# Performance work log

Measured on AMD Instinct MI355X. Metric: run time of the kernel, lower is better.

Reference implementation:

```python
import jax, jax.numpy as jnp
import numpy as np

P, H, T, B = 16, 24, 168, 4096


def _lstm(x, W_ih, W_hh, b_ih, b_hh):
    # x: [B, T, F]; PyTorch gate order i, f, g, o; returns all hidden states [B, T, H]
    Bsz = x.shape[0]
    Hd = W_hh.shape[1]
    # batch the input GEMM over all timesteps
    xg = jnp.einsum('btf,gf->btg', x, W_ih) + b_ih + b_hh  # [B, T, 4H]

    def step(carry, xt):
        h, c = carry
        g = xt + h @ W_hh.T  # [B, 4H]
        i, f, gg, o = jnp.split(g, 4, axis=-1)
        c = jax.nn.sigmoid(f) * c + jax.nn.sigmoid(i) * jnp.tanh(gg)
        h = jax.nn.sigmoid(o) * jnp.tanh(c)
        return (h, c), h

    h0 = jnp.zeros((Bsz, Hd), x.dtype)
    _, hs = jax.lax.scan(step, (h0, h0), jnp.swapaxes(xg, 0, 1))
    return jnp.swapaxes(hs, 0, 1)  # [B, T, H]


def setup_inputs() -> dict:
    key = jax.random.key(0)
    ks = jax.random.split(key, 14)
    s1 = 1.0 / np.sqrt(H)
    u = lambda k, shape: jax.random.uniform(k, shape, jnp.float32, -s1, s1)
    return {
        'x': jax.random.normal(ks[0], (B, T, P), jnp.float32),
        'W_ih1': u(ks[1], (4 * H, P)), 'W_hh1': u(ks[2], (4 * H, H)),
        'b_ih1': u(ks[3], (4 * H,)), 'b_hh1': u(ks[4], (4 * H,)),
        'W_ih2': u(ks[5], (4 * H, H)), 'W_hh2': u(ks[6], (4 * H, H)),
        'b_ih2': u(ks[7], (4 * H,)), 'b_hh2': u(ks[8], (4 * H,)),
        'W1': u(ks[9], (16, H)), 'b1': u(ks[10], (16,)),
        'W2': u(ks[11], (H, 16)), 'b2': u(ks[12], (H,)),
    }


def reference(x, W_ih1, W_hh1, b_ih1, b_hh1, W_ih2, W_hh2, b_ih2, b_hh2, W1, b1, W2, b2):
    h = jnp.tanh(_lstm(x, W_ih1, W_hh1, b_ih1, b_hh1))       # [B, T, H]
    h = jnp.tanh(_lstm(h, W_ih2, W_hh2, b_ih2, b_hh2))       # [B, T, H]
    h = h[:, -1, :]                                           # [B, H]
    h = jax.nn.relu(h @ W1.T + b1)                            # [B, 16]; dropout = identity (eval mode)
    out = h @ W2.T + b2                                       # [B, 24]
    return out.reshape(out.shape[0], -1, 1)                   # [B, 24, 1]
```

## Files before the change

### kernel.cpp

```cpp
#include <hip/hip_runtime.h>

constexpr int T = 168;
constexpr int P = 16;
constexpr int H = 24;

typedef float v2f __attribute__((ext_vector_type(2)));

__device__ __forceinline__ v2f mk2(float a, float b) { v2f r; r[0] = a; r[1] = b; return r; }
__device__ __forceinline__ v2f bc2(float a)          { v2f r; r[0] = a; r[1] = a; return r; }
__device__ __forceinline__ v2f pkfma(v2f a, v2f b, v2f c) {
    return __builtin_elementwise_fma(a, b, c);
}

__device__ __forceinline__ float rcp_f(float x) { return __builtin_amdgcn_rcpf(x); }
__device__ __forceinline__ float sigm_f(float x) { return rcp_f(1.f + __expf(-x)); }
__device__ __forceinline__ float tanh_fast(float x) {
    return fmaf(2.f, rcp_f(1.f + __expf(-2.f * x)), -1.f);
}

#define KEEP2(v) asm volatile("" : "+v"(v))
#define LDS_SYNC() asm volatile("s_waitcnt lgkmcnt(0)" ::: "memory")

__global__ __attribute__((amdgpu_flat_work_group_size(64, 64),
                          amdgpu_waves_per_eu(2, 2)))
void lstm2_pk(const float* __restrict__ x,
              const float* __restrict__ Wih1, const float* __restrict__ Whh1,
              const float* __restrict__ bih1, const float* __restrict__ bhh1,
              const float* __restrict__ Wih2, const float* __restrict__ Whh2,
              const float* __restrict__ bih2, const float* __restrict__ bhh2,
              const float* __restrict__ W1, const float* __restrict__ b1,
              const float* __restrict__ W2, const float* __restrict__ b2,
              float* __restrict__ out)
{
    const int lane = threadIdx.x;
    const int s    = (lane < 48) ? lane : 47;
    const int u    = s % H;
    const int half = s / H;
    const int q0   = half * H + u;
    const int q1   = (2 + half) * H + u;
    const int rowA = blockIdx.x * 2;
    const int rowB = rowA + 1;

    v2f wx[P];
    v2f wh[H];
    v2f vx[H];
    v2f vh[H];
    #pragma unroll
    for (int k = 0; k < P; ++k) wx[k] = mk2(Wih1[q0 * P + k], Wih1[q1 * P + k]);
    #pragma unroll
    for (int k = 0; k < H; ++k) wh[k] = mk2(Whh1[q0 * H + k], Whh1[q1 * H + k]);
    #pragma unroll
    for (int k = 0; k < H; ++k) vx[k] = mk2(Wih2[q0 * H + k], Wih2[q1 * H + k]);
    #pragma unroll
    for (int k = 0; k < H; ++k) vh[k] = mk2(Whh2[q0 * H + k], Whh2[q1 * H + k]);
    v2f bias1 = mk2(bih1[q0] + bhh1[q0], bih1[q1] + bhh1[q1]);
    v2f bias2 = mk2(bih2[q0] + bhh2[q0], bih2[q1] + bhh2[q1]);

    #pragma unroll
    for (int k = 0; k < P; ++k) KEEP2(wx[k]);
    #pragma unroll
    for (int k = 0; k < H; ++k) { KEEP2(wh[k]); KEEP2(vx[k]); KEEP2(vh[k]); }
    KEEP2(bias1); KEEP2(bias2);

    __shared__ __align__(16) float h1s[2][32];
    __shared__ __align__(16) float t1s[2][32];
    __shared__ __align__(16) float h2s[2][32];

    if (lane < H) {
        h1s[0][lane] = 0.f; t1s[0][lane] = 0.f; h2s[0][lane] = 0.f;
        h1s[1][lane] = 0.f; t1s[1][lane] = 0.f; h2s[1][lane] = 0.f;
    }
    LDS_SYNC();

    const float* __restrict__ xA = x + (size_t)rowA * T * P;
    const float* __restrict__ xB = x + (size_t)rowB * T * P;

    float c1A = 0.f, c2A = 0.f, c1B = 0.f, c2B = 0.f;

    for (int t = 0; t < T; ++t) {
        v2f gA = bias1, gB = bias1;
        #pragma unroll
        for (int k = 0; k < P; ++k) {
            gA = pkfma(bc2(xA[t * P + k]), wx[k], gA);
            gB = pkfma(bc2(xB[t * P + k]), wx[k], gB);
        }
        #pragma unroll
        for (int k = 0; k < H / 4; ++k) {
            float4 ha = ((const float4*)h1s[0])[k];
            float4 hb = ((const float4*)h1s[1])[k];
            gA = pkfma(bc2(ha.x), wh[4*k],   gA);  gB = pkfma(bc2(hb.x), wh[4*k],   gB);
            gA = pkfma(bc2(ha.y), wh[4*k+1], gA);  gB = pkfma(bc2(hb.y), wh[4*k+1], gB);
            gA = pkfma(bc2(ha.z), wh[4*k+2], gA);  gB = pkfma(bc2(hb.z), wh[4*k+2], gB);
            gA = pkfma(bc2(ha.w), wh[4*k+3], gA);  gB = pkfma(bc2(hb.w), wh[4*k+3], gB);
        }
        {
            float a0 = sigm_f(gA[0]);
            float px = (half == 0) ? gA[1] + gA[1] : gA[1];
            float sv = sigm_f(px);
            float a1 = (half == 0) ? sv + sv - 1.f : sv;
            float fa = __shfl(a0, lane + 24);
            float oa = __shfl(a1, lane + 24);
            c1A = fmaf(fa, c1A, a0 * a1);
            float hv = oa * tanh_fast(c1A);
            float th = tanh_fast(hv);
            if (lane < H) { h1s[0][lane] = hv; t1s[0][lane] = th; }
        }
        {
            float a0 = sigm_f(gB[0]);
            float px = (half == 0) ? gB[1] + gB[1] : gB[1];
            float sv = sigm_f(px);
            float a1 = (half == 0) ? sv + sv - 1.f : sv;
            float fa = __shfl(a0, lane + 24);
            float oa = __shfl(a1, lane + 24);
            c1B = fmaf(fa, c1B, a0 * a1);
            float hv = oa * tanh_fast(c1B);
            float th = tanh_fast(hv);
            if (lane < H) { h1s[1][lane] = hv; t1s[1][lane] = th; }
        }
        LDS_SYNC();

        v2f fA = bias2, fB = bias2;
        #pragma unroll
        for (int k = 0; k < H / 4; ++k) {
            float4 ta = ((const float4*)t1s[0])[k];
            float4 tb = ((const float4*)t1s[1])[k];
            fA = pkfma(bc2(ta.x), vx[4*k],   fA);  fB = pkfma(bc2(tb.x), vx[4*k],   fB);
            fA = pkfma(bc2(ta.y), vx[4*k+1], fA);  fB = pkfma(bc2(tb.y), vx[4*k+1], fB);
            fA = pkfma(bc2(ta.z), vx[4*k+2], fA);  fB = pkfma(bc2(tb.z), vx[4*k+2], fB);
            fA = pkfma(bc2(ta.w), vx[4*k+3], fA);  fB = pkfma(bc2(tb.w), vx[4*k+3], fB);
        }
        #pragma unroll
        for (int k = 0; k < H / 4; ++k) {
            float4 ha = ((const float4*)h2s[0])[k];
            float4 hb = ((const float4*)h2s[1])[k];
            fA = pkfma(bc2(ha.x), vh[4*k],   fA);  fB = pkfma(bc2(hb.x), vh[4*k],   fB);
            fA = pkfma(bc2(ha.y), vh[4*k+1], fA);  fB = pkfma(bc2(hb.y), vh[4*k+1], fB);
            fA = pkfma(bc2(ha.z), vh[4*k+2], fA);  fB = pkfma(bc2(hb.z), vh[4*k+2], fB);
            fA = pkfma(bc2(ha.w), vh[4*k+3], fA);  fB = pkfma(bc2(hb.w), vh[4*k+3], fB);
        }
        {
            float a2 = sigm_f(fA[0]);
            float py = (half == 0) ? fA[1] + fA[1] : fA[1];
            float sw = sigm_f(py);
            float a3 = (half == 0) ? sw + sw - 1.f : sw;
            float fb = __shfl(a2, lane + 24);
            float ob = __shfl(a3, lane + 24);
            c2A = fmaf(fb, c2A, a2 * a3);
            if (lane < H) h2s[0][lane] = ob * tanh_fast(c2A);
        }
        {
            float a2 = sigm_f(fB[0]);
            float py = (half == 0) ? fB[1] + fB[1] : fB[1];
            float sw = sigm_f(py);
            float a3 = (half == 0) ? sw + sw - 1.f : sw;
            float fb = __shfl(a2, lane + 24);
            float ob = __shfl(a3, lane + 24);
            c2B = fmaf(fb, c2B, a2 * a3);
            if (lane < H) h2s[1][lane] = ob * tanh_fast(c2B);
        }
        LDS_SYNC();
    }

    if (lane < H) {
        t1s[0][lane] = tanh_fast(h2s[0][lane]);
        t1s[1][lane] = tanh_fast(h2s[1][lane]);
    }
    LDS_SYNC();
    if (lane < 16) {
        float accA = b1[lane], accB = b1[lane];
        #pragma unroll
        for (int j = 0; j < H; ++j) {
            float w = W1[lane * H + j];
            accA = fmaf(t1s[0][j], w, accA);
            accB = fmaf(t1s[1][j], w, accB);
        }
        h1s[0][lane] = fmaxf(accA, 0.f);
        h1s[1][lane] = fmaxf(accB, 0.f);
    }
    LDS_SYNC();
    if (lane < H) {
        float accA = b2[lane], accB = b2[lane];
        #pragma unroll
        for (int j = 0; j < 16; ++j) {
            float w = W2[lane * 16 + j];
            accA = fmaf(h1s[0][j], w, accA);
            accB = fmaf(h1s[1][j], w, accB);
        }
        out[(size_t)rowA * H + lane] = accA;
        out[(size_t)rowB * H + lane] = accB;
    }
}

extern "C" void kernel_launch(void* const* d_in, const int* in_sizes, int n_in,
                              void* d_out, int out_size, void* d_ws, size_t ws_size,
                              hipStream_t stream)
{
    const float* x    = (const float*)d_in[0];
    const float* Wih1 = (const float*)d_in[1];
    const float* Whh1 = (const float*)d_in[2];
    const float* bih1 = (const float*)d_in[3];
    const float* bhh1 = (const float*)d_in[4];
    const float* Wih2 = (const float*)d_in[5];
    const float* Whh2 = (const float*)d_in[6];
    const float* bih2 = (const float*)d_in[7];
    const float* bhh2 = (const float*)d_in[8];
    const float* W1   = (const float*)d_in[9];
    const float* b1   = (const float*)d_in[10];
    const float* W2   = (const float*)d_in[11];
    const float* b2   = (const float*)d_in[12];
    float* out = (float*)d_out;

    const int B = in_sizes[0] / (T * P);
    hipLaunchKernelGGL(lstm2_pk, dim3(B / 2), dim3(64), 0, stream,
                       x, Wih1, Whh1, bih1, bhh1, Wih2, Whh2, bih2, bhh2,
                       W1, b1, W2, b2, out);
}
```

Measured before the change: 389.4 us.

## Use permlane32 swap for gate exchange and prefetch x rows into registers

Lanes are remapped so the two wave halves hold i/g and f/o gates. Gate products are exchanged with permlane32_swap instead of __shfl, and each half reads its own LDS row and swaps to get the other row, which halves LDS reads. The explicit lgkmcnt waits inside the timestep loop are replaced by compiler-only fences, and the next timestep's x values are prefetched into registers during layer 2. Dropping the waits relies on in-order LDS behaviour within a wave and on compiler-inserted waits, which is a correctness risk.

```diff
diff --git a/kernel.cpp b/kernel.cpp
--- a/kernel.cpp
+++ b/kernel.cpp
@@ -19,32 +19,60 @@
 }
 
 #define KEEP2(v) asm volatile("" : "+v"(v))
+#define SCHED_FENCE() asm volatile("" ::: "memory")
 #define LDS_SYNC() asm volatile("s_waitcnt lgkmcnt(0)" ::: "memory")
+
+#define HAVE_PLSWAP __has_builtin(__builtin_amdgcn_permlane32_swap)
+__device__ __forceinline__ void swap32(float v, float& lowdup, float& updup) {
+#if HAVE_PLSWAP
+    auto r = __builtin_amdgcn_permlane32_swap(__float_as_uint(v), __float_as_uint(v),
+                                              false, false);
+    lowdup = __uint_as_float(r[0]);
+    updup  = __uint_as_float(r[1]);
+#else
+    int o = __shfl(__float_as_int(v), (int)(threadIdx.x & 63) ^ 32);
+    float ov = __int_as_float(o);
+    bool lo = ((threadIdx.x & 63) < 32);
+    lowdup = lo ? v : ov;
+    updup  = lo ? ov : v;
+#endif
+}
+
+__device__ __forceinline__ void quad_both(const float* myrow, const float* row0,
+                                          const float* row1, int k,
+                                          float4& qa, float4& qb) {
+#if HAVE_PLSWAP
+    float4 q = ((const float4*)myrow)[k];
+    swap32(q.x, qa.x, qb.x);
+    swap32(q.y, qa.y, qb.y);
+    swap32(q.z, qa.z, qb.z);
+    swap32(q.w, qa.w, qb.w);
+#else
+    qa = ((const float4*)row0)[k];
+    qb = ((const float4*)row1)[k];
+#endif
+}
 
 __global__ __attribute__((amdgpu_flat_work_group_size(64, 64),
                           amdgpu_waves_per_eu(2, 2)))
-void lstm2_pk(const float* __restrict__ x,
-              const float* __restrict__ Wih1, const float* __restrict__ Whh1,
-              const float* __restrict__ bih1, const float* __restrict__ bhh1,
-              const float* __restrict__ Wih2, const float* __restrict__ Whh2,
-              const float* __restrict__ bih2, const float* __restrict__ bhh2,
-              const float* __restrict__ W1, const float* __restrict__ b1,
-              const float* __restrict__ W2, const float* __restrict__ b2,
-              float* __restrict__ out)
+void lstm2_swp(const float* __restrict__ x,
+               const float* __restrict__ Wih1, const float* __restrict__ Whh1,
+               const float* __restrict__ bih1, const float* __restrict__ bhh1,
+               const float* __restrict__ Wih2, const float* __restrict__ Whh2,
+               const float* __restrict__ bih2, const float* __restrict__ bhh2,
+               const float* __restrict__ W1, const float* __restrict__ b1,
+               const float* __restrict__ W2, const float* __restrict__ b2,
+               float* __restrict__ out)
 {
-    const int lane = threadIdx.x;
-    const int s    = (lane < 48) ? lane : 47;
-    const int u    = s % H;
-    const int half = s / H;
-    const int q0   = half * H + u;
-    const int q1   = (2 + half) * H + u;
-    const int rowA = blockIdx.x * 2;
-    const int rowB = rowA + 1;
-
-    v2f wx[P];
-    v2f wh[H];
-    v2f vx[H];
-    v2f vh[H];
+    const int lane  = threadIdx.x & 63;
+    const int inner = lane & 31;
+    const int half  = lane >> 5;
+    const int u     = (inner < 24) ? inner : inner - 8;
+    const int q0    = half ? H + u     : u;
+    const int q1    = half ? 3 * H + u : 2 * H + u;
+    const int rowA  = blockIdx.x * 2;
+
+    v2f wx[P], wh[H], vx[H], vh[H];
     #pragma unroll
     for (int k = 0; k < P; ++k) wx[k] = mk2(Wih1[q0 * P + k], Wih1[q1 * P + k]);
     #pragma unroll
@@ -55,7 +83,6 @@
     for (int k = 0; k < H; ++k) vh[k] = mk2(Whh2[q0 * H + k], Whh2[q1 * H + k]);
     v2f bias1 = mk2(bih1[q0] + bhh1[q0], bih1[q1] + bhh1[q1]);
     v2f bias2 = mk2(bih2[q0] + bhh2[q0], bih2[q1] + bhh2[q1]);
-
     #pragma unroll
     for (int k = 0; k < P; ++k) KEEP2(wx[k]);
     #pragma unroll
@@ -65,65 +92,70 @@
     __shared__ __align__(16) float h1s[2][32];
     __shared__ __align__(16) float t1s[2][32];
     __shared__ __align__(16) float h2s[2][32];
-
-    if (lane < H) {
-        h1s[0][lane] = 0.f; t1s[0][lane] = 0.f; h2s[0][lane] = 0.f;
-        h1s[1][lane] = 0.f; t1s[1][lane] = 0.f; h2s[1][lane] = 0.f;
-    }
-    LDS_SYNC();
+    __shared__ __align__(16) float hd [2][16];
+
+    if (inner < 24) { h1s[half][inner] = 0.f; h2s[half][inner] = 0.f; }
+    SCHED_FENCE();
 
     const float* __restrict__ xA = x + (size_t)rowA * T * P;
-    const float* __restrict__ xB = x + (size_t)rowB * T * P;
-
-    float c1A = 0.f, c2A = 0.f, c1B = 0.f, c2B = 0.f;
+    const float* __restrict__ xB = x + (size_t)(rowA + 1) * T * P;
+
+    float4 sxA[4], sxB[4];
+    #pragma unroll
+    for (int j = 0; j < 4; ++j) { sxA[j] = ((const float4*)xA)[j]; sxB[j] = ((const float4*)xB)[j]; }
+
+    const float* mh1 = &h1s[half][0];
+    const float* mt1 = &t1s[half][0];
+    const float* mh2 = &h2s[half][0];
+
+    float c1A = 0.f, c1B = 0.f, c2A = 0.f, c2B = 0.f;
 
     for (int t = 0; t < T; ++t) {
         v2f gA = bias1, gB = bias1;
         #pragma unroll
-        for (int k = 0; k < P; ++k) {
-            gA = pkfma(bc2(xA[t * P + k]), wx[k], gA);
-            gB = pkfma(bc2(xB[t * P + k]), wx[k], gB);
-        }
-        #pragma unroll
-        for (int k = 0; k < H / 4; ++k) {
-            float4 ha = ((const float4*)h1s[0])[k];
-            float4 hb = ((const float4*)h1s[1])[k];
+        for (int j = 0; j < 4; ++j) {
+            gA = pkfma(bc2(sxA[j].x), wx[4*j],   gA);  gB = pkfma(bc2(sxB[j].x), wx[4*j],   gB);
+            gA = pkfma(bc2(sxA[j].y), wx[4*j+1], gA);  gB = pkfma(bc2(sxB[j].y), wx[4*j+1], gB);
+            gA = pkfma(bc2(sxA[j].z), wx[4*j+2], gA);  gB = pkfma(bc2(sxB[j].z), wx[4*j+2], gB);
+            gA = pkfma(bc2(sxA[j].w), wx[4*j+3], gA);  gB = pkfma(bc2(sxB[j].w), wx[4*j+3], gB);
+        }
+        #pragma unroll
+        for (int k = 0; k < H / 4; ++k) {
+            float4 ha, hb;
+            quad_both(mh1, &h1s[0][0], &h1s[1][0], k, ha, hb);
             gA = pkfma(bc2(ha.x), wh[4*k],   gA);  gB = pkfma(bc2(hb.x), wh[4*k],   gB);
             gA = pkfma(bc2(ha.y), wh[4*k+1], gA);  gB = pkfma(bc2(hb.y), wh[4*k+1], gB);
             gA = pkfma(bc2(ha.z), wh[4*k+2], gA);  gB = pkfma(bc2(hb.z), wh[4*k+2], gB);
             gA = pkfma(bc2(ha.w), wh[4*k+3], gA);  gB = pkfma(bc2(hb.w), wh[4*k+3], gB);
         }
-        {
-            float a0 = sigm_f(gA[0]);
-            float px = (half == 0) ? gA[1] + gA[1] : gA[1];
-            float sv = sigm_f(px);
-            float a1 = (half == 0) ? sv + sv - 1.f : sv;
-            float fa = __shfl(a0, lane + 24);
-            float oa = __shfl(a1, lane + 24);
-            c1A = fmaf(fa, c1A, a0 * a1);
-            float hv = oa * tanh_fast(c1A);
-            float th = tanh_fast(hv);
-            if (lane < H) { h1s[0][lane] = hv; t1s[0][lane] = th; }
-        }
-        {
-            float a0 = sigm_f(gB[0]);
-            float px = (half == 0) ? gB[1] + gB[1] : gB[1];
-            float sv = sigm_f(px);
-            float a1 = (half == 0) ? sv + sv - 1.f : sv;
-            float fa = __shfl(a0, lane + 24);
-            float oa = __shfl(a1, lane + 24);
-            c1B = fmaf(fa, c1B, a0 * a1);
-            float hv = oa * tanh_fast(c1B);
-            float th = tanh_fast(hv);
-            if (lane < H) { h1s[1][lane] = hv; t1s[1][lane] = th; }
-        }
-        LDS_SYNC();
+        float a0A = sigm_f(gA[0]);
+        float pxA = half ? gA[1] : gA[1] + gA[1];
+        float svA = sigm_f(pxA);
+        float a1A = half ? svA : svA + svA - 1.f;
+        float a0B = sigm_f(gB[0]);
+        float pxB = half ? gB[1] : gB[1] + gB[1];
+        float svB = sigm_f(pxB);
+        float a1B = half ? svB : svB + svB - 1.f;
+        float pA_lo, pA_up, pB_lo, pB_up;
+        swap32(a0A * a1A, pA_lo, pA_up);
+        swap32(a0B * a1B, pB_lo, pB_up);
+        c1A = fmaf(a0A, c1A, pA_lo);
+        c1B = fmaf(a0B, c1B, pB_lo);
+        float hvA = a1A * tanh_fast(c1A);
+        float hvB = a1B * tanh_fast(c1B);
+        float thA = tanh_fast(hvA);
+        float thB = tanh_fast(hvB);
+        if (half == 1 && inner < 24) {
+            h1s[0][inner] = hvA;  h1s[1][inner] = hvB;
+            t1s[0][inner] = thA;  t1s[1][inner] = thB;
+        }
+        SCHED_FENCE();
 
         v2f fA = bias2, fB = bias2;
         #pragma unroll
         for (int k = 0; k < H / 4; ++k) {
-            float4 ta = ((const float4*)t1s[0])[k];
-            float4 tb = ((const float4*)t1s[1])[k];
+            float4 ta, tb;
+            quad_both(mt1, &t1s[0][0], &t1s[1][0], k, ta, tb);
             fA = pkfma(bc2(ta.x), vx[4*k],   fA);  fB = pkfma(bc2(tb.x), vx[4*k],   fB);
             fA = pkfma(bc2(ta.y), vx[4*k+1], fA);  fB = pkfma(bc2(tb.y), vx[4*k+1], fB);
             fA = pkfma(bc2(ta.z), vx[4*k+2], fA);  fB = pkfma(bc2(tb.z), vx[4*k+2], fB);
@@ -131,63 +163,76 @@
         }
         #pragma unroll
         for (int k = 0; k < H / 4; ++k) {
-            float4 ha = ((const float4*)h2s[0])[k];
-            float4 hb = ((const float4*)h2s[1])[k];
+            float4 ha, hb;
+            quad_both(mh2, &h2s[0][0], &h2s[1][0], k, ha, hb);
             fA = pkfma(bc2(ha.x), vh[4*k],   fA);  fB = pkfma(bc2(hb.x), vh[4*k],   fB);
             fA = pkfma(bc2(ha.y), vh[4*k+1], fA);  fB = pkfma(bc2(hb.y), vh[4*k+1], fB);
             fA = pkfma(bc2(ha.z), vh[4*k+2], fA);  fB = pkfma(bc2(hb.z), vh[4*k+2], fB);
             fA = pkfma(bc2(ha.w), vh[4*k+3], fA);  fB = pkfma(bc2(hb.w), vh[4*k+3], fB);
         }
         {
-            float a2 = sigm_f(fA[0]);
-            float py = (half == 0) ? fA[1] + fA[1] : fA[1];
-            float sw = sigm_f(py);
-            float a3 = (half == 0) ? sw + sw - 1.f : sw;
-            float fb = __shfl(a2, lane + 24);
-            float ob = __shfl(a3, lane + 24);
-            c2A = fmaf(fb, c2A, a2 * a3);
-            if (lane < H) h2s[0][lane] = ob * tanh_fast(c2A);
-        }
-        {
-            float a2 = sigm_f(fB[0]);
-            float py = (half == 0) ? fB[1] + fB[1] : fB[1];
-            float sw = sigm_f(py);
-            float a3 = (half == 0) ? sw + sw - 1.f : sw;
-            float fb = __shfl(a2, lane + 24);
-            float ob = __shfl(a3, lane + 24);
-            c2B = fmaf(fb, c2B, a2 * a3);
-            if (lane < H) h2s[1][lane] = ob * tanh_fast(c2B);
-        }
-        LDS_SYNC();
+            int tn = (t + 1 < T) ? t + 1 : t;
+            const float4* pA4 = (const float4*)(xA + (size_t)tn * P);
+            const float4* pB4 = (const float4*)(xB + (size_t)tn * P);
+            #pragma unroll
+            for (int j = 0; j < 4; ++j) { sxA[j] = pA4[j]; sxB[j] = pB4[j]; }
+        }
+        float b0A = sigm_f(fA[0]);
+        float qxA = half ? fA[1] : fA[1] + fA[1];
+        float swA = sigm_f(qxA);
+        float b1Av = half ? swA : swA + swA - 1.f;
+        float b0B = sigm_f(fB[0]);
+        float qxB = half ? fB[1] : fB[1] + fB[1];
+        float swB = sigm_f(qxB);
+        float b1Bv = half ? swB : swB + swB - 1.f;
+        float rA_lo, rA_up, rB_lo, rB_up;
+        swap32(b0A * b1Av, rA_lo, rA_up);
+        swap32(b0B * b1Bv, rB_lo, rB_up);
+        c2A = fmaf(b0A, c2A, rA_lo);
+        c2B = fmaf(b0B, c2B, rB_lo);
+        float h2A = b1Av * tanh_fast(c2A);
+        float h2B = b1Bv * tanh_fast(c2B);
+        if (half == 1 && inner < 24) {
+            h2s[0][inner] = h2A;  h2s[1][inner] = h2B;
+        }
+        SCHED_FENCE();
     }
 
-    if (lane < H) {
-        t1s[0][lane] = tanh_fast(h2s[0][lane]);
-        t1s[1][lane] = tanh_fast(h2s[1][lane]);
+    LDS_SYNC();
+
+    if (inner < 24) t1s[half][inner] = tanh_fast(h2s[half][inner]);
+    SCHED_FENCE();
+    {
+        const int l16 = inner & 15;
+        float w1r[H];
+        #pragma unroll
+        for (int j = 0; j < H; ++j) w1r[j] = W1[l16 * H + j];
+        float acc = b1[l16];
+        #pragma unroll
+        for (int k = 0; k < H / 4; ++k) {
+            float4 q = ((const float4*)&t1s[half][0])[k];
+            acc = fmaf(q.x, w1r[4*k],   acc);
+            acc = fmaf(q.y, w1r[4*k+1], acc);
+            acc = fmaf(q.z, w1r[4*k+2], acc);
+            acc = fmaf(q.w, w1r[4*k+3], acc);
+        }
+        if (inner < 16) hd[half][inner] = fmaxf(acc, 0.f);
     }
-    LDS_SYNC();
-    if (lane < 16) {
-        float accA = b1[lane], accB = b1[lane];
-        #pragma unroll
-        for (int j = 0; j < H; ++j) {
-            float w = W1[lane * H + j];
-            accA = fmaf(t1s[0][j], w, accA);
-            accB = fmaf(t1s[1][j], w, accB);
-        }
-        h1s[0][lane] = fmaxf(accA, 0.f);
-        h1s[1][lane] = fmaxf(accB, 0.f);
-    }
-    LDS_SYNC();
-    if (lane < H) {
-        float accA = b2[lane], accB = b2[lane];
-        #pragma unroll
-        for (int j = 0; j < 16; ++j) {
-            float w = W2[lane * 16 + j];
-            accA = fmaf(h1s[0][j], w, accA);
-            accB = fmaf(h1s[1][j], w, accB);
-        }
-        out[(size_t)rowA * H + lane] = accA;
-        out[(size_t)rowB * H + lane] = accB;
+    SCHED_FENCE();
+    {
+        float w2r[16];
+        #pragma unroll
+        for (int j = 0; j < 16; ++j) w2r[j] = W2[u * 16 + j];
+        float acc = b2[u];
+        #pragma unroll
+        for (int k = 0; k < 4; ++k) {
+            float4 q = ((const float4*)&hd[half][0])[k];
+            acc = fmaf(q.x, w2r[4*k],   acc);
+            acc = fmaf(q.y, w2r[4*k+1], acc);
+            acc = fmaf(q.z, w2r[4*k+2], acc);
+            acc = fmaf(q.w, w2r[4*k+3], acc);
+        }
+        if (inner < 24) out[(size_t)(rowA + half) * H + inner] = acc;
     }
 }
 
@@ -211,7 +256,7 @@
     float* out = (float*)d_out;
 
     const int B = in_sizes[0] / (T * P);
-    hipLaunchKernelGGL(lstm2_pk, dim3(B / 2), dim3(64), 0, stream,
+    hipLaunchKernelGGL(lstm2_swp, dim3(B / 2), dim3(64), 0, stream,
                        x, Wih1, Whh1, bih1, bhh1, Wih2, Whh2, bih2, bhh2,
                        W1, b1, W2, b2, out);
 }
```

Measured after the change: 499.3 us. 28.2% more time.
